# Performance work log

Hardware: AMD Instinct MI355X
Metric: run time of the kernel (lower is better)

Reference implementation:

```python
import jax, jax.numpy as jnp
import numpy as np

B, S, E = 4, 4096, 1024
H = 16
D = E // H  # head_dim = 64


def setup_inputs() -> dict:
    key = jax.random.key(0)
    kx, kk, kq, kv = jax.random.split(key, 4)
    scale = 1.0 / np.sqrt(E)
    return {
        "x": jax.random.normal(kx, (B, S, E), dtype=jnp.float32),
        # torch nn.Linear weight shape: [out_features, in_features] = [D, E]
        "Wk": jax.random.uniform(kk, (D, E), dtype=jnp.float32, minval=-scale, maxval=scale),
        "Wq": jax.random.uniform(kq, (D, E), dtype=jnp.float32, minval=-scale, maxval=scale),
        "Wv": jax.random.uniform(kv, (D, E), dtype=jnp.float32, minval=-scale, maxval=scale),
    }


def reference(x, Wk, Wq, Wv):
    # Projections: x @ W^T  -> [B, S, D]
    k = jnp.einsum('bse,de->bsd', x, Wk)
    q = jnp.einsum('bse,de->bsd', x, Wq)
    v = jnp.einsum('bse,de->bsd', x, Wv)
    # Scaled scores [B, S, S]
    scores = jnp.einsum('bqd,bkd->bqk', q, k) * (D ** -0.5)
    # Causal mask: position q attends to k <= q
    causal = jnp.tril(jnp.ones((S, S), dtype=bool))
    scores = jnp.where(causal, scores, -jnp.inf)
    attn = jax.nn.softmax(scores, axis=-1)
    # dropout omitted (eval mode / attn_pdrop=0)
    out = jnp.einsum('bqk,bkd->bqd', attn, v)
    return out
```

## Files before the change

kernel.cpp:

```cpp
#include <hip/hip_runtime.h>
#include <hip/hip_bf16.h>
#include <stdint.h>

#define BB 4
#define SS 4096
#define EE 1024
#define DD 64

typedef __attribute__((ext_vector_type(8))) short short8;
typedef __attribute__((ext_vector_type(4))) float f32x4;

__device__ inline uint32_t cvtpk(float lo, float hi) {
    uint32_t r;
    asm("v_cvt_pk_bf16_f32 %0, %1, %2" : "=v"(r) : "v"(lo), "v"(hi));
    return r;
}
__device__ inline float bf2f_lo(uint32_t u) {
    union { uint32_t u; float f; } v; v.u = u << 16; return v.f;
}
__device__ inline float bf2f_hi(uint32_t u) {
    union { uint32_t u; float f; } v; v.u = u & 0xFFFF0000u; return v.f;
}

#define GL16(g, l) __builtin_amdgcn_global_load_lds( \
    (const __attribute__((address_space(1))) void*)(g), \
    (__attribute__((address_space(3))) void*)(l), 16, 0, 0)

__global__ __launch_bounds__(256) void wconv_kernel(
    const float* __restrict__ Wq, const float* __restrict__ Wk,
    const float* __restrict__ Wv, ushort* __restrict__ Wb)
{
    int tid = blockIdx.x * 256 + threadIdx.x;
    int sel = tid >> 13;
    int off = (tid & 8191) * 8;
    const float* src = (sel == 0) ? Wq : ((sel == 1) ? Wk : Wv);
    float4 a = *reinterpret_cast<const float4*>(src + off);
    float4 b = *reinterpret_cast<const float4*>(src + off + 4);
    uint4 o;
    o.x = cvtpk(a.x, a.y); o.y = cvtpk(a.z, a.w);
    o.z = cvtpk(b.x, b.y); o.w = cvtpk(b.z, b.w);
    *reinterpret_cast<uint4*>(Wb + (size_t)sel * 65536 + off) = o;
}

__global__ __launch_bounds__(256) void proj_kernel(
    const float* __restrict__ x, const ushort* __restrict__ Wb,
    ushort* __restrict__ q_ws, ushort* __restrict__ k_ws, ushort* __restrict__ vT_ws)
{
    __shared__ __align__(16) char smem[3 * 12288];
    const int t = threadIdx.x;
    const int wid = t >> 6, lane = t & 63, g = lane >> 4, lr = lane & 15;
    const int sel = blockIdx.x >> 8;
    const int m0 = (blockIdx.x & 255) * 64;
    const int NT = EE / 32;

    f32x4 acc[4];
#pragma unroll
    for (int i = 0; i < 4; ++i) acc[i] = (f32x4)(0.0f);

#define PSTAGE(KT, BUFI) do { \
    char* xb_ = smem + (BUFI) * 12288; \
    char* wb_ = xb_ + 8192; \
    int e0_ = (KT) * 32; \
    _Pragma("unroll") \
    for (int i = 0; i < 2; ++i) { \
        int v = i * 256 + t; int row = v >> 3, c = v & 7; \
        GL16(&x[(size_t)(m0 + row) * EE + e0_ + ((c ^ (row & 7)) << 2)], xb_ + v * 16); \
    } \
    { \
        int v = t; int row = v >> 2, u = v & 3; \
        GL16(&Wb[(size_t)(sel * 64 + row) * EE + e0_ + ((u ^ (row & 3)) << 3)], wb_ + v * 16); \
    } \
} while (0)

    PSTAGE(0, 0); PSTAGE(1, 1); PSTAGE(2, 2);

    for (int kt = 0; kt < NT; ++kt) {
        asm volatile("s_waitcnt vmcnt(6)" ::: "memory");
        __builtin_amdgcn_s_barrier();
        __builtin_amdgcn_sched_barrier(0);

        const char* xb = smem + (kt % 3) * 12288;
        const char* wb = xb + 8192;

        short8 af[4];
#pragma unroll
        for (int ni = 0; ni < 4; ++ni) {
            int row = ni * 16 + lr;
            af[ni] = *reinterpret_cast<const short8*>(wb + row * 64 + ((g ^ (lr & 3)) << 4));
        }
        short8 bfr;
        {
            int row = wid * 16 + lr;
            int u0 = (2 * g) ^ (lr & 7);
            f32x4 lo = *reinterpret_cast<const f32x4*>(xb + row * 128 + u0 * 16);
            f32x4 hi = *reinterpret_cast<const f32x4*>(xb + row * 128 + (u0 ^ 1) * 16);
            union { short8 s; uint32_t u[4]; } p;
            p.u[0] = cvtpk(lo[0], lo[1]); p.u[1] = cvtpk(lo[2], lo[3]);
            p.u[2] = cvtpk(hi[0], hi[1]); p.u[3] = cvtpk(hi[2], hi[3]);
            bfr = p.s;
        }
#pragma unroll
        for (int ni = 0; ni < 4; ++ni)
            acc[ni] = __builtin_amdgcn_mfma_f32_16x16x32_bf16(af[ni], bfr, acc[ni], 0, 0, 0);

        asm volatile("s_waitcnt lgkmcnt(0)" ::: "memory");
        __builtin_amdgcn_sched_barrier(0);
        __builtin_amdgcn_s_barrier();
        __builtin_amdgcn_sched_barrier(0);

        int nx = (kt + 3 < NT) ? kt + 3 : NT - 1;
        PSTAGE(nx, kt % 3);
    }

    const int m = m0 + wid * 16 + lr;
    const int b = m >> 12, s = m & (SS - 1);
#pragma unroll
    for (int ni = 0; ni < 4; ++ni) {
        int d0 = ni * 16 + 4 * g;
        uint2 p;
        p.x = cvtpk(acc[ni][0], acc[ni][1]);
        p.y = cvtpk(acc[ni][2], acc[ni][3]);
        if (sel == 0) {
            *reinterpret_cast<uint2*>(q_ws + ((size_t)b * SS + s) * DD + d0) = p;
        } else if (sel == 1) {
            *reinterpret_cast<uint2*>(k_ws + ((size_t)b * SS + s) * DD + d0) = p;
        } else {
            vT_ws[((size_t)b * DD + d0 + 0) * SS + s] = (ushort)(p.x & 0xFFFF);
            vT_ws[((size_t)b * DD + d0 + 1) * SS + s] = (ushort)(p.x >> 16);
            vT_ws[((size_t)b * DD + d0 + 2) * SS + s] = (ushort)(p.y & 0xFFFF);
            vT_ws[((size_t)b * DD + d0 + 3) * SS + s] = (ushort)(p.y >> 16);
        }
    }
}

__global__ __launch_bounds__(512) void attn_kernel(
    const ushort* __restrict__ q_ws, const ushort* __restrict__ k_ws,
    const ushort* __restrict__ vT_ws, uint32_t* __restrict__ pO32,
    float* __restrict__ pml)
{
    __shared__ __align__(16) char kv_lds[2][32768];
    const int t = threadIdx.x;
    const int wid = t >> 6, lane = t & 63, g = lane >> 4, lr = lane & 15;
    const int bid = blockIdx.x;
    const int f = bid & 3;
    const int b = (bid >> 2) & 3;
    const int qblk = 31 - (bid >> 4);
    const int qb_w = qblk * 128 + wid * 16;

    const ushort* qp = q_ws + ((size_t)b * SS + qb_w + lr) * DD;
    short8 qf0 = *reinterpret_cast<const short8*>(qp + g * 8);
    short8 qf1 = *reinterpret_cast<const short8*>(qp + 32 + g * 8);

    float l_r = 0.0f;
    f32x4 acc[4];
#pragma unroll
    for (int i = 0; i < 4; ++i) acc[i] = (f32x4)(0.0f);

    const float sc = 0.125f * 1.44269504f;
    const float MB = 5.770780164f;
    const int nt = qblk + 1;
    const int nfull = ((qb_w - 127) >> 7) + 1;
    const int cs = (nt + 3) >> 2;
    const int t0 = f * cs;
    const int t1 = min(nt, (f + 1) * cs);
    const ushort* kbase = k_ws + (size_t)b * SS * DD;
    const ushort* vbase = vT_ws + (size_t)b * DD * SS;

    const int s0 = g & 1, hi = g >> 1;
    const int idxA = ((lr + 16 * ((s0 << 1) | hi)) << 2);
    const int idxB = idxA ^ 128;

#define ASTAGE(KT, BUFI) do { \
    char* kb_ = kv_lds[BUFI]; \
    int kv0_ = (KT) * 128; \
    _Pragma("unroll") \
    for (int i = 0; i < 2; ++i) { \
        int v = i * 512 + t; int row = v >> 3, c = v & 7; \
        GL16(kbase + (size_t)(kv0_ + row) * DD + ((c ^ (row & 7)) << 3), kb_ + v * 16); \
    } \
    _Pragma("unroll") \
    for (int i = 0; i < 2; ++i) { \
        int v = i * 512 + t; int row = v >> 4, c = v & 15; \
        GL16(vbase + (size_t)row * SS + kv0_ + ((c ^ ((row & 7) << 1)) << 3), kb_ + 16384 + v * 16); \
    } \
} while (0)

    if (t0 < t1) {
        ASTAGE(t0, 0);
        ASTAGE((t0 + 1 < t1) ? t0 + 1 : t0, 1);

        for (int kt = t0; kt < t1; ++kt) {
            const int cur = (kt - t0) & 1;
            asm volatile("s_waitcnt vmcnt(4)" ::: "memory");
            __builtin_amdgcn_s_barrier();
            __builtin_amdgcn_sched_barrier(0);

            const char* kb = kv_lds[cur];
            const char* vb = kb + 16384;
            const int kv0 = kt * 128;

            f32x4 sfr[8];
            __builtin_amdgcn_s_setprio(1);
#pragma unroll
            for (int nf = 0; nf < 8; ++nf) {
                int row = nf * 16 + lr;
                short8 b0 = *reinterpret_cast<const short8*>(kb + row * 128 + ((g ^ (row & 7)) << 4));
                short8 b1 = *reinterpret_cast<const short8*>(kb + row * 128 + (((4 + g) ^ (row & 7)) << 4));
                f32x4 s_ = (f32x4)(0.0f);
                s_ = __builtin_amdgcn_mfma_f32_16x16x32_bf16(b0, qf0, s_, 0, 0, 0);
                s_ = __builtin_amdgcn_mfma_f32_16x16x32_bf16(b1, qf1, s_, 0, 0, 0);
                sfr[nf] = s_;
            }
            __builtin_amdgcn_s_setprio(0);

            if (kt >= nfull) {
#pragma unroll
                for (int nf = 0; nf < 8; ++nf)
#pragma unroll
                    for (int jr = 0; jr < 4; ++jr)
                        if (kv0 + nf * 16 + 4 * g + jr > qb_w + lr) sfr[nf][jr] = -1e30f;
            }

            float ps = 0.0f;
            uint32_t pk[16];
#pragma unroll
            for (int nf = 0; nf < 8; ++nf) {
                float e0_ = exp2f(fmaf(sfr[nf][0], sc, -MB));
                float e1_ = exp2f(fmaf(sfr[nf][1], sc, -MB));
                float e2_ = exp2f(fmaf(sfr[nf][2], sc, -MB));
                float e3_ = exp2f(fmaf(sfr[nf][3], sc, -MB));
                ps += (e0_ + e1_) + (e2_ + e3_);
                pk[nf * 2 + 0] = cvtpk(e0_, e1_);
                pk[nf * 2 + 1] = cvtpk(e2_, e3_);
            }
            l_r += ps;

            uint32_t pw[4][4];
#pragma unroll
            for (int cc = 0; cc < 4; ++cc) {
                uint32_t r0 = (uint32_t)__builtin_amdgcn_ds_permute(idxA, (int)(s0 ? pk[cc * 4 + 2] : pk[cc * 4 + 0]));
                uint32_t r1 = (uint32_t)__builtin_amdgcn_ds_permute(idxA, (int)(s0 ? pk[cc * 4 + 3] : pk[cc * 4 + 1]));
                uint32_t r2 = (uint32_t)__builtin_amdgcn_ds_permute(idxB, (int)(s0 ? pk[cc * 4 + 0] : pk[cc * 4 + 2]));
                uint32_t r3 = (uint32_t)__builtin_amdgcn_ds_permute(idxB, (int)(s0 ? pk[cc * 4 + 1] : pk[cc * 4 + 3]));
                pw[cc][0] = hi ? r2 : r0;
                pw[cc][1] = hi ? r3 : r1;
                pw[cc][2] = hi ? r0 : r2;
                pw[cc][3] = hi ? r1 : r3;
            }

            __builtin_amdgcn_s_setprio(1);
#pragma unroll
            for (int cc = 0; cc < 4; ++cc) {
                union { uint32_t u[4]; short8 s; } pb;
                pb.u[0] = pw[cc][0]; pb.u[1] = pw[cc][1];
                pb.u[2] = pw[cc][2]; pb.u[3] = pw[cc][3];
#pragma unroll
                for (int df = 0; df < 4; ++df) {
                    int row = df * 16 + lr;
                    short8 vb_ = *reinterpret_cast<const short8*>(
                        vb + row * 256 + (((cc * 4 + g) ^ ((row & 7) << 1)) << 4));
                    acc[df] = __builtin_amdgcn_mfma_f32_16x16x32_bf16(vb_, pb.s, acc[df], 0, 0, 0);
                }
            }
            __builtin_amdgcn_s_setprio(0);

            asm volatile("s_waitcnt lgkmcnt(0)" ::: "memory");
            __builtin_amdgcn_sched_barrier(0);
            __builtin_amdgcn_s_barrier();
            __builtin_amdgcn_sched_barrier(0);

            int nx = (kt + 2 < t1) ? kt + 2 : t1 - 1;
            ASTAGE(nx, cur);
        }
    }

    l_r += __shfl_xor(l_r, 16);
    l_r += __shfl_xor(l_r, 32);
    const int pidx = ((b * 256 + qblk * 8 + wid) * 4 + f);
    uint32_t* po = pO32 + (size_t)pidx * 512;
#pragma unroll
    for (int df = 0; df < 4; ++df) {
        po[(df * 8 + 2 * g + 0) * 16 + lr] = cvtpk(acc[df][0], acc[df][1]);
        po[(df * 8 + 2 * g + 1) * 16 + lr] = cvtpk(acc[df][2], acc[df][3]);
    }
    if (g == 0) pml[(size_t)pidx * 16 + lr] = l_r;
}

__global__ __launch_bounds__(64) void combine_kernel(
    const uint32_t* __restrict__ pO32, const float* __restrict__ pml,
    float* __restrict__ out)
{
    const int t = threadIdx.x;
    const int q = t & 15, dblk = t >> 4;
    const int grp = blockIdx.x;
    const int b = grp >> 8, qt = grp & 255;
    const int qb = qt * 16;

    float l = 0.0f;
#pragma unroll
    for (int f = 0; f < 4; ++f) l += pml[(size_t)(grp * 4 + f) * 16 + q];

    float o[16];
#pragma unroll
    for (int i = 0; i < 16; ++i) o[i] = 0.0f;
#pragma unroll
    for (int f = 0; f < 4; ++f) {
        const uint32_t* src = pO32 + (size_t)(grp * 4 + f) * 512 + dblk * 128 + q;
#pragma unroll
        for (int r0 = 0; r0 < 8; ++r0) {
            uint32_t u = src[r0 * 16];
            o[2 * r0 + 0] += bf2f_lo(u);
            o[2 * r0 + 1] += bf2f_hi(u);
        }
    }
    float inv = 1.0f / l;
    float* op = out + ((size_t)b * SS + qb + q) * DD + dblk * 16;
#pragma unroll
    for (int i = 0; i < 4; ++i) {
        float4 st;
        st.x = o[4 * i + 0] * inv; st.y = o[4 * i + 1] * inv;
        st.z = o[4 * i + 2] * inv; st.w = o[4 * i + 3] * inv;
        *reinterpret_cast<float4*>(op + 4 * i) = st;
    }
}

extern "C" void kernel_launch(void* const* d_in, const int* in_sizes, int n_in,
                              void* d_out, int out_size, void* d_ws, size_t ws_size,
                              hipStream_t stream) {
    const float* x  = (const float*)d_in[0];
    const float* Wk = (const float*)d_in[1];
    const float* Wq = (const float*)d_in[2];
    const float* Wv = (const float*)d_in[3];
    ushort* q_ws  = (ushort*)d_ws;
    ushort* k_ws  = q_ws + (size_t)BB * SS * DD;
    ushort* vT_ws = k_ws + (size_t)BB * SS * DD;
    ushort* Wb    = vT_ws + (size_t)BB * SS * DD;
    uint32_t* pO32 = (uint32_t*)(Wb + 192 * 1024);
    float* pml     = (float*)(pO32 + (size_t)4096 * 512);
    float* out = (float*)d_out;

    hipLaunchKernelGGL(wconv_kernel, dim3(96), dim3(256), 0, stream, Wq, Wk, Wv, Wb);
    hipLaunchKernelGGL(proj_kernel, dim3(768), dim3(256), 0, stream,
                       x, Wb, q_ws, k_ws, vT_ws);
    hipLaunchKernelGGL(attn_kernel, dim3(BB * 32 * 4), dim3(512), 0, stream,
                       q_ws, k_ws, vT_ws, pO32, pml);
    hipLaunchKernelGGL(combine_kernel, dim3(BB * SS / 16), dim3(64), 0, stream,
                       pO32, pml, out);
}
```

Baseline: 62.19 us.

## Rewrite projection GEMM to load directly from global and cover 96 output columns per block

The projection kernel drops its triple-buffered LDS pipeline and reads x rows and bf16 weights straight from global memory into MFMA operands. Each block now computes 96 of the 192 fused Q/K/V output columns instead of 64 columns of one projection, so x is read twice across the grid rather than three times. The grid shrinks from 768 to 512 blocks. This trades LDS staging and barriers for uncoalesced-ish direct global loads that rely on cache, and adds a vmcnt(0) wait before the attention kernel's epilogue.

```diff
diff --git a/kernel.cpp b/kernel.cpp
--- a/kernel.cpp
+++ b/kernel.cpp
@@ -46,77 +46,39 @@
     const float* __restrict__ x, const ushort* __restrict__ Wb,
     ushort* __restrict__ q_ws, ushort* __restrict__ k_ws, ushort* __restrict__ vT_ws)
 {
-    __shared__ __align__(16) char smem[3 * 12288];
     const int t = threadIdx.x;
     const int wid = t >> 6, lane = t & 63, g = lane >> 4, lr = lane & 15;
-    const int sel = blockIdx.x >> 8;
-    const int m0 = (blockIdx.x & 255) * 64;
-    const int NT = EE / 32;
-
-    f32x4 acc[4];
-#pragma unroll
-    for (int i = 0; i < 4; ++i) acc[i] = (f32x4)(0.0f);
-
-#define PSTAGE(KT, BUFI) do { \
-    char* xb_ = smem + (BUFI) * 12288; \
-    char* wb_ = xb_ + 8192; \
-    int e0_ = (KT) * 32; \
-    _Pragma("unroll") \
-    for (int i = 0; i < 2; ++i) { \
-        int v = i * 256 + t; int row = v >> 3, c = v & 7; \
-        GL16(&x[(size_t)(m0 + row) * EE + e0_ + ((c ^ (row & 7)) << 2)], xb_ + v * 16); \
-    } \
-    { \
-        int v = t; int row = v >> 2, u = v & 3; \
-        GL16(&Wb[(size_t)(sel * 64 + row) * EE + e0_ + ((u ^ (row & 3)) << 3)], wb_ + v * 16); \
-    } \
-} while (0)
-
-    PSTAGE(0, 0); PSTAGE(1, 1); PSTAGE(2, 2);
-
-    for (int kt = 0; kt < NT; ++kt) {
-        asm volatile("s_waitcnt vmcnt(6)" ::: "memory");
-        __builtin_amdgcn_s_barrier();
-        __builtin_amdgcn_sched_barrier(0);
-
-        const char* xb = smem + (kt % 3) * 12288;
-        const char* wb = xb + 8192;
-
-        short8 af[4];
-#pragma unroll
-        for (int ni = 0; ni < 4; ++ni) {
-            int row = ni * 16 + lr;
-            af[ni] = *reinterpret_cast<const short8*>(wb + row * 64 + ((g ^ (lr & 3)) << 4));
+    const int m0 = (blockIdx.x >> 1) * 64;
+    const int nh = blockIdx.x & 1;
+
+    const int m = m0 + wid * 16 + lr;
+    const float* xrow = x + (size_t)m * EE;
+    const ushort* wb0 = Wb + (size_t)(nh * 96 + lr) * EE;
+
+    f32x4 acc[6];
+#pragma unroll
+    for (int i = 0; i < 6; ++i) acc[i] = (f32x4)(0.0f);
+
+#pragma unroll 2
+    for (int kt = 0; kt < 32; ++kt) {
+        const int e0 = kt * 32;
+        float4 xlo = *reinterpret_cast<const float4*>(xrow + e0 + g * 8);
+        float4 xhi = *reinterpret_cast<const float4*>(xrow + e0 + g * 8 + 4);
+        union { short8 s; uint32_t u[4]; } bp;
+        bp.u[0] = cvtpk(xlo.x, xlo.y); bp.u[1] = cvtpk(xlo.z, xlo.w);
+        bp.u[2] = cvtpk(xhi.x, xhi.y); bp.u[3] = cvtpk(xhi.z, xhi.w);
+#pragma unroll
+        for (int ni = 0; ni < 6; ++ni) {
+            short8 af = *reinterpret_cast<const short8*>(wb0 + (size_t)ni * 16 * EE + e0 + g * 8);
+            acc[ni] = __builtin_amdgcn_mfma_f32_16x16x32_bf16(af, bp.s, acc[ni], 0, 0, 0);
         }
-        short8 bfr;
-        {
-            int row = wid * 16 + lr;
-            int u0 = (2 * g) ^ (lr & 7);
-            f32x4 lo = *reinterpret_cast<const f32x4*>(xb + row * 128 + u0 * 16);
-            f32x4 hi = *reinterpret_cast<const f32x4*>(xb + row * 128 + (u0 ^ 1) * 16);
-            union { short8 s; uint32_t u[4]; } p;
-            p.u[0] = cvtpk(lo[0], lo[1]); p.u[1] = cvtpk(lo[2], lo[3]);
-            p.u[2] = cvtpk(hi[0], hi[1]); p.u[3] = cvtpk(hi[2], hi[3]);
-            bfr = p.s;
-        }
-#pragma unroll
-        for (int ni = 0; ni < 4; ++ni)
-            acc[ni] = __builtin_amdgcn_mfma_f32_16x16x32_bf16(af[ni], bfr, acc[ni], 0, 0, 0);
-
-        asm volatile("s_waitcnt lgkmcnt(0)" ::: "memory");
-        __builtin_amdgcn_sched_barrier(0);
-        __builtin_amdgcn_s_barrier();
-        __builtin_amdgcn_sched_barrier(0);
-
-        int nx = (kt + 3 < NT) ? kt + 3 : NT - 1;
-        PSTAGE(nx, kt % 3);
-    }
-
-    const int m = m0 + wid * 16 + lr;
+    }
+
     const int b = m >> 12, s = m & (SS - 1);
 #pragma unroll
-    for (int ni = 0; ni < 4; ++ni) {
-        int d0 = ni * 16 + 4 * g;
+    for (int ni = 0; ni < 6; ++ni) {
+        int n0 = nh * 96 + ni * 16 + 4 * g;
+        int sel = n0 >> 6, d0 = n0 & 63;
         uint2 p;
         p.x = cvtpk(acc[ni][0], acc[ni][1]);
         p.y = cvtpk(acc[ni][2], acc[ni][3]);
@@ -273,6 +235,7 @@
             ASTAGE(nx, cur);
         }
     }
+    asm volatile("s_waitcnt vmcnt(0)" ::: "memory");
 
     l_r += __shfl_xor(l_r, 16);
     l_r += __shfl_xor(l_r, 32);
@@ -340,7 +303,7 @@
     float* out = (float*)d_out;
 
     hipLaunchKernelGGL(wconv_kernel, dim3(96), dim3(256), 0, stream, Wq, Wk, Wv, Wb);
-    hipLaunchKernelGGL(proj_kernel, dim3(768), dim3(256), 0, stream,
+    hipLaunchKernelGGL(proj_kernel, dim3(512), dim3(256), 0, stream,
                        x, Wb, q_ws, k_ws, vT_ws);
     hipLaunchKernelGGL(attn_kernel, dim3(BB * 32 * 4), dim3(512), 0, stream,
                        q_ws, k_ws, vT_ws, pO32, pml);
```

Result: slower. 99.64 us (+60.2%).
